# Kernel tuning notes

Measured on AMD Instinct MI355X. Metric: run time of the kernel, lower is better.

## Reference

```python
import jax, jax.numpy as jnp
import numpy as np

B, T, HID = 2, 2048, 2048
NH, DK, DV = 6, 256, 512
KEY_DIM, VAL_DIM = NH * DK, NH * DV
CONV = 4
EPS = 1e-5
SCALE = DK ** -0.5


def setup_inputs() -> dict:
    ks = jax.random.split(jax.random.key(0), 14)
    g = lambda k, shape, s=1.0: jax.random.normal(k, shape, jnp.float32) * s
    # dt_bias init as in the module: inv_dt = dt + log(-expm1(-dt))
    dt = jnp.exp(jax.random.uniform(ks[12], (NH,), jnp.float32)
                 * (np.log(0.1) - np.log(0.001)) + np.log(0.001))
    dt = jnp.clip(dt, 1e-4, None)
    inv_dt = dt + jnp.log(-jnp.expm1(-dt))
    return {
        "hidden_states": g(ks[0], (B, T, HID)),
        "w_q": g(ks[1], (HID, KEY_DIM), HID ** -0.5),
        "w_k": g(ks[2], (HID, KEY_DIM), HID ** -0.5),
        "w_v": g(ks[3], (HID, VAL_DIM), HID ** -0.5),
        "w_a": g(ks[4], (HID, NH), HID ** -0.5),
        "w_b": g(ks[5], (HID, NH), HID ** -0.5),
        "w_g": g(ks[6], (HID, VAL_DIM), HID ** -0.5),
        "w_o": g(ks[7], (VAL_DIM, HID), VAL_DIM ** -0.5),
        "conv_q": g(ks[8], (KEY_DIM, CONV), CONV ** -0.5),
        "conv_k": g(ks[9], (KEY_DIM, CONV), CONV ** -0.5),
        "conv_v": g(ks[10], (VAL_DIM, CONV), CONV ** -0.5),
        "A_log": jnp.log(jax.random.uniform(ks[11], (NH,), jnp.float32, 1e-3, 16.0)),
        "dt_bias": inv_dt,
        "norm_w": jnp.ones((DV,), jnp.float32),
    }


def short_conv(x, w):
    # depthwise causal conv1d, kernel size CONV, followed by SiLU
    K = w.shape[1]
    xp = jnp.pad(x, ((0, 0), (K - 1, 0), (0, 0)))  # left pad (causal)
    out = sum(xp[:, j:j + x.shape[1], :] * w[:, j] for j in range(K))
    return jax.nn.silu(out)


def l2norm(x):
    n = jnp.sqrt(jnp.sum(x * x, axis=-1, keepdims=True))
    return x / jnp.maximum(n, 1e-6)


def gated_delta_rule(q, k, v, glog, beta):
    # q,k: [B,T,H,DK]; v: [B,T,H,DV]; glog,beta: [B,T,H]
    # S_t = exp(g_t) (I - b_t k_t k_t^T) S_{t-1} + b_t k_t v_t^T ; o_t = scale * q_t^T S_t
    tm = lambda x: jnp.moveaxis(x, 1, 0)  # time-major

    def step(S, xs):  # S: [B,H,DK,DV]
        qt, kt, vt, gt, bt = xs
        Sd = jnp.exp(gt)[..., None, None] * S
        kS = jnp.einsum('bhk,bhkv->bhv', kt, Sd)           # k^T (a S)
        u = bt[..., None] * (vt - kS)                       # [B,H,DV]
        S_new = Sd + kt[..., None] * u[:, :, None, :]       # rank-1 update
        ot = SCALE * jnp.einsum('bhk,bhkv->bhv', qt, S_new)
        return S_new, ot

    S0 = jnp.zeros((B, NH, DK, DV), q.dtype)
    _, o = jax.lax.scan(step, S0, (tm(q), tm(k), tm(v), tm(glog), tm(beta)))
    return jnp.moveaxis(o, 0, 1)  # [B,T,H,DV]


def reference(hidden_states, w_q, w_k, w_v, w_a, w_b, w_g, w_o,
              conv_q, conv_k, conv_v, A_log, dt_bias, norm_w):
    x = hidden_states
    q = short_conv(x @ w_q, conv_q).reshape(B, T, NH, DK)
    k = short_conv(x @ w_k, conv_k).reshape(B, T, NH, DK)
    v = short_conv(x @ w_v, conv_v).reshape(B, T, NH, DV)
    beta = jax.nn.sigmoid(x @ w_b)                          # [B,T,H]
    glog = -jnp.exp(A_log) * jax.nn.softplus(x @ w_a + dt_bias)
    q = l2norm(q)
    k = l2norm(k)
    o = gated_delta_rule(q, k, v, glog, beta)               # [B,T,H,DV]
    # gated RMSNorm: rmsnorm(o) * w * silu(g_out)
    g_out = (x @ w_g).reshape(B, T, NH, DV)
    o = o * jax.lax.rsqrt(jnp.mean(o * o, axis=-1, keepdims=True) + EPS)
    o = o * norm_w * jax.nn.silu(g_out)
    return o.reshape(B, T, VAL_DIM) @ w_o
```

## Files before the change

### kernel.cpp

```cpp
#include <hip/hip_runtime.h>
#include <hip/hip_bf16.h>
#include <cstdint>

#define B_ 2
#define T_ 2048
#define HID 2048
#define NH 6
#define DK 256
#define DV 512
#define KEY_DIM (NH*DK)
#define VAL_DIM (NH*DV)
#define EPS_ 1e-5f
#define SCALE_ 0.0625f
#define MT (B_*T_)
#define CC 64
#define NC (T_/CC)

typedef __attribute__((ext_vector_type(8))) short short8;
typedef __attribute__((ext_vector_type(4))) float floatx4;
typedef __attribute__((ext_vector_type(4))) unsigned int uint4v;

union Pk8 { unsigned short us[8]; uint4v v; };

__device__ inline unsigned short f32_to_bf16(float f) {
    union { float f; unsigned int u; } v; v.f = f;
    unsigned int u = v.u;
    u += 0x7fffu + ((u >> 16) & 1u);
    return (unsigned short)(u >> 16);
}

__device__ inline float bf16_to_f32(unsigned short u) {
    union { unsigned int u; float f; } v; v.u = ((unsigned int)u) << 16;
    return v.f;
}

__device__ inline float silu_f(float x) { return x / (1.f + expf(-x)); }

__global__ __launch_bounds__(256) void cvt_bf16_kernel(const float* __restrict__ in,
                                                       unsigned short* __restrict__ out, int n) {
    int i = (blockIdx.x * 256 + threadIdx.x) * 4;
    if (i >= n) return;
    float4 v = *reinterpret_cast<const float4*>(in + i);
    ushort4 o;
    o.x = f32_to_bf16(v.x); o.y = f32_to_bf16(v.y);
    o.z = f32_to_bf16(v.z); o.w = f32_to_bf16(v.w);
    *reinterpret_cast<ushort4*>(out + i) = o;
}

__global__ __launch_bounds__(256) void transpose_cvt_kernel(const float* __restrict__ in,
                                                            unsigned short* __restrict__ out,
                                                            int K, int N) {
    __shared__ float tile[64][65];
    int k0 = blockIdx.x * 64, n0 = blockIdx.y * 64;
    int r = threadIdx.x >> 2, c0 = (threadIdx.x & 3) * 16;
    const float* src = in + (size_t)(k0 + r) * N + n0 + c0;
#pragma unroll
    for (int j = 0; j < 16; j += 4) {
        float4 v = *reinterpret_cast<const float4*>(src + j);
        tile[r][c0 + j + 0] = v.x; tile[r][c0 + j + 1] = v.y;
        tile[r][c0 + j + 2] = v.z; tile[r][c0 + j + 3] = v.w;
    }
    __syncthreads();
    int n = threadIdx.x >> 2, kc = (threadIdx.x & 3) * 16;
    unsigned short* dst = out + (size_t)(n0 + n) * K + k0 + kc;
#pragma unroll
    for (int j = 0; j < 16; j += 4) {
        ushort4 o;
        o.x = f32_to_bf16(tile[kc + j + 0][n]);
        o.y = f32_to_bf16(tile[kc + j + 1][n]);
        o.z = f32_to_bf16(tile[kc + j + 2][n]);
        o.w = f32_to_bf16(tile[kc + j + 3][n]);
        *reinterpret_cast<ushort4*>(dst + j) = o;
    }
}

#define BM 128
#define BN 128
#define BK 32
#define LDS_S 40

__global__ __launch_bounds__(256) void gemm_bf16_kernel(const unsigned short* __restrict__ A,
                                                        const unsigned short* __restrict__ BT,
                                                        float* __restrict__ C,
                                                        int M, int N, int K) {
    __shared__ __align__(16) unsigned short As[BM * LDS_S];
    __shared__ __align__(16) unsigned short Bs[BN * LDS_S];
    int tid = threadIdx.x;
    int m0 = blockIdx.y * BM, n0 = blockIdx.x * BN;
    int wave = tid >> 6, lane = tid & 63;
    int wr = (wave >> 1) * 64, wc = (wave & 1) * 64;
    int l15 = lane & 15, lh = lane >> 4;

    int srow = tid >> 1, shalf = tid & 1;
    const unsigned short* agp = A + (size_t)(m0 + srow) * K + shalf * 16;
    const unsigned short* bgp = BT + (size_t)(n0 + srow) * K + shalf * 16;
    unsigned short* asl = As + srow * LDS_S + shalf * 16;
    unsigned short* bsl = Bs + srow * LDS_S + shalf * 16;

    floatx4 acc[4][4];
#pragma unroll
    for (int m = 0; m < 4; m++)
#pragma unroll
        for (int n = 0; n < 4; n++) acc[m][n] = (floatx4){0.f, 0.f, 0.f, 0.f};

    for (int kt = 0; kt < K; kt += BK) {
        uint4v av0 = *reinterpret_cast<const uint4v*>(agp + kt);
        uint4v av1 = *reinterpret_cast<const uint4v*>(agp + kt + 8);
        uint4v bv0 = *reinterpret_cast<const uint4v*>(bgp + kt);
        uint4v bv1 = *reinterpret_cast<const uint4v*>(bgp + kt + 8);
        __syncthreads();
        *reinterpret_cast<uint4v*>(asl) = av0;
        *reinterpret_cast<uint4v*>(asl + 8) = av1;
        *reinterpret_cast<uint4v*>(bsl) = bv0;
        *reinterpret_cast<uint4v*>(bsl + 8) = bv1;
        __syncthreads();
        short8 a[4], b[4];
#pragma unroll
        for (int i = 0; i < 4; i++)
            a[i] = *reinterpret_cast<const short8*>(As + (wr + i * 16 + l15) * LDS_S + lh * 8);
#pragma unroll
        for (int i = 0; i < 4; i++)
            b[i] = *reinterpret_cast<const short8*>(Bs + (wc + i * 16 + l15) * LDS_S + lh * 8);
#pragma unroll
        for (int m = 0; m < 4; m++)
#pragma unroll
            for (int n = 0; n < 4; n++)
                acc[m][n] = __builtin_amdgcn_mfma_f32_16x16x32_bf16(a[m], b[n], acc[m][n], 0, 0, 0);
    }

#pragma unroll
    for (int m = 0; m < 4; m++)
#pragma unroll
        for (int n = 0; n < 4; n++) {
            int row = m0 + wr + m * 16 + lh * 4;
            int col = n0 + wc + n * 16 + l15;
#pragma unroll
            for (int j = 0; j < 4; j++)
                C[(size_t)(row + j) * N + col] = acc[m][n][j];
        }
}

__global__ __launch_bounds__(256) void ab_kernel(const float* __restrict__ x,
                                                 const float* __restrict__ wa,
                                                 const float* __restrict__ wb,
                                                 const float* __restrict__ A_log,
                                                 const float* __restrict__ dtb,
                                                 float* __restrict__ glog,
                                                 float* __restrict__ beta) {
    int bt = blockIdx.x, tid = threadIdx.x;
    const float* xr = x + (size_t)bt * HID;
    float pa[NH], pb[NH];
#pragma unroll
    for (int h = 0; h < NH; h++) { pa[h] = 0.f; pb[h] = 0.f; }
    for (int k = tid; k < HID; k += 256) {
        float xv = xr[k];
#pragma unroll
        for (int h = 0; h < NH; h++) {
            pa[h] = fmaf(xv, wa[k * NH + h], pa[h]);
            pb[h] = fmaf(xv, wb[k * NH + h], pb[h]);
        }
    }
    __shared__ float red[256][12];
#pragma unroll
    for (int h = 0; h < NH; h++) { red[tid][h] = pa[h]; red[tid][NH + h] = pb[h]; }
    __syncthreads();
    for (int s = 128; s > 0; s >>= 1) {
        if (tid < s)
#pragma unroll
            for (int j = 0; j < 12; j++) red[tid][j] += red[tid + s][j];
        __syncthreads();
    }
    if (tid < NH) {
        float a = red[0][tid] + dtb[tid];
        float sp = (a > 20.f) ? a : log1pf(expf(a));
        glog[(size_t)bt * NH + tid] = -expf(A_log[tid]) * sp;
        float bv = red[0][NH + tid];
        beta[(size_t)bt * NH + tid] = 1.f / (1.f + expf(-bv));
    }
}

__global__ __launch_bounds__(256) void conv_silu_l2norm_kernel(const float* __restrict__ in,
                                                               const float* __restrict__ w,
                                                               float* __restrict__ out) {
    int bt = blockIdx.x;
    int h = blockIdx.y;
    int t = bt & (T_ - 1);
    int c = h * DK + threadIdx.x;
    float4 wv = *reinterpret_cast<const float4*>(w + (size_t)c * 4);
    float acc = 0.f;
    if (t >= 3) {
        acc = in[(size_t)(bt - 3) * KEY_DIM + c] * wv.x
            + in[(size_t)(bt - 2) * KEY_DIM + c] * wv.y
            + in[(size_t)(bt - 1) * KEY_DIM + c] * wv.z
            + in[(size_t)(bt) * KEY_DIM + c] * wv.w;
    } else {
        if (t - 3 >= 0) acc = fmaf(in[(size_t)(bt - 3) * KEY_DIM + c], wv.x, acc);
        if (t - 2 >= 0) acc = fmaf(in[(size_t)(bt - 2) * KEY_DIM + c], wv.y, acc);
        if (t - 1 >= 0) acc = fmaf(in[(size_t)(bt - 1) * KEY_DIM + c], wv.z, acc);
        acc = fmaf(in[(size_t)bt * KEY_DIM + c], wv.w, acc);
    }
    float s = silu_f(acc);
    float ss = s * s;
#pragma unroll
    for (int m = 1; m < 64; m <<= 1) ss += __shfl_xor(ss, m);
    __shared__ float wsum[4];
    if ((threadIdx.x & 63) == 0) wsum[threadIdx.x >> 6] = ss;
    __syncthreads();
    float tot = wsum[0] + wsum[1] + wsum[2] + wsum[3];
    float r = 1.f / fmaxf(sqrtf(tot), 1e-6f);
    out[(size_t)bt * KEY_DIM + c] = s * r;
}

__global__ __launch_bounds__(256) void conv_silu_kernel(const float* __restrict__ in,
                                                        const float* __restrict__ w,
                                                        float* __restrict__ out) {
    int bt = blockIdx.x;
    int c = blockIdx.y * 256 + threadIdx.x;
    int t = bt & (T_ - 1);
    float4 wv = *reinterpret_cast<const float4*>(w + (size_t)c * 4);
    float acc = 0.f;
    if (t >= 3) {
        acc = in[(size_t)(bt - 3) * VAL_DIM + c] * wv.x
            + in[(size_t)(bt - 2) * VAL_DIM + c] * wv.y
            + in[(size_t)(bt - 1) * VAL_DIM + c] * wv.z
            + in[(size_t)(bt) * VAL_DIM + c] * wv.w;
    } else {
        if (t - 3 >= 0) acc = fmaf(in[(size_t)(bt - 3) * VAL_DIM + c], wv.x, acc);
        if (t - 2 >= 0) acc = fmaf(in[(size_t)(bt - 2) * VAL_DIM + c], wv.y, acc);
        if (t - 1 >= 0) acc = fmaf(in[(size_t)(bt - 1) * VAL_DIM + c], wv.z, acc);
        acc = fmaf(in[(size_t)bt * VAL_DIM + c], wv.w, acc);
    }
    out[(size_t)bt * VAL_DIM + c] = silu_f(acc);
}

__global__ __launch_bounds__(256) void chunk_prep_kernel(
    const float* __restrict__ QC, const float* __restrict__ KC, const float* __restrict__ VC,
    const float* __restrict__ GL, const float* __restrict__ BE,
    unsigned short* __restrict__ Qg, unsigned short* __restrict__ KB,
    unsigned short* __restrict__ KlT, unsigned short* __restrict__ Tm,
    unsigned short* __restrict__ Am, unsigned short* __restrict__ BVT,
    float* __restrict__ gend) {
    int c = blockIdx.x;
    int bh = blockIdx.y;
    int b = bh / NH, h = bh % NH;
    size_t idx = (size_t)bh * NC + c;
    int bt0 = b * T_ + c * CC;

    __shared__ __align__(16) char ldsbuf[64 * 264 * 2 * 2];
    unsigned short* Kb = (unsigned short*)ldsbuf;
    unsigned short* Qb = (unsigned short*)(ldsbuf + 33792);
    float* Vst = (float*)ldsbuf;
    float* Msf = (float*)(ldsbuf + 33792);
    unsigned short* Ts_lds = (unsigned short*)(ldsbuf + 50432);
    __shared__ float gc[64], es[64], bb_s[64], gtmp[64];

    int tid = threadIdx.x, wave = tid >> 6, lane = tid & 63;
    int l15 = lane & 15, lh = lane >> 4;

    if (tid < 64) {
        gtmp[tid] = GL[(size_t)(bt0 + tid) * NH + h];
        bb_s[tid] = BE[(size_t)(bt0 + tid) * NH + h];
    }

    {
        int r = tid >> 2, seg = (tid & 3) * 64;
        const float* ksrc = KC + (size_t)(bt0 + r) * KEY_DIM + h * DK + seg;
        const float* qsrc = QC + (size_t)(bt0 + r) * KEY_DIM + h * DK + seg;
#pragma unroll
        for (int jj = 0; jj < 8; jj++) {
            float4 a = *reinterpret_cast<const float4*>(ksrc + jj * 8);
            float4 a2 = *reinterpret_cast<const float4*>(ksrc + jj * 8 + 4);
            Pk8 pk;
            pk.us[0] = f32_to_bf16(a.x);  pk.us[1] = f32_to_bf16(a.y);
            pk.us[2] = f32_to_bf16(a.z);  pk.us[3] = f32_to_bf16(a.w);
            pk.us[4] = f32_to_bf16(a2.x); pk.us[5] = f32_to_bf16(a2.y);
            pk.us[6] = f32_to_bf16(a2.z); pk.us[7] = f32_to_bf16(a2.w);
            *reinterpret_cast<uint4v*>(Kb + r * 264 + seg + jj * 8) = pk.v;
            float4 qa = *reinterpret_cast<const float4*>(qsrc + jj * 8);
            float4 qa2 = *reinterpret_cast<const float4*>(qsrc + jj * 8 + 4);
            pk.us[0] = f32_to_bf16(qa.x);  pk.us[1] = f32_to_bf16(qa.y);
            pk.us[2] = f32_to_bf16(qa.z);  pk.us[3] = f32_to_bf16(qa.w);
            pk.us[4] = f32_to_bf16(qa2.x); pk.us[5] = f32_to_bf16(qa2.y);
            pk.us[6] = f32_to_bf16(qa2.z); pk.us[7] = f32_to_bf16(qa2.w);
            *reinterpret_cast<uint4v*>(Qb + r * 264 + seg + jj * 8) = pk.v;
        }
    }
    __syncthreads();

    if (wave == 0) {
        float xg = gtmp[lane];
#pragma unroll
        for (int off = 1; off < 64; off <<= 1) {
            float yg = __shfl_up(xg, off, 64);
            if (lane >= off) xg += yg;
        }
        gc[lane] = xg;
    }

    floatx4 kkf[4], qkf[4];
#pragma unroll
    for (int nt = 0; nt < 4; nt++) { kkf[nt] = (floatx4){0,0,0,0}; qkf[nt] = (floatx4){0,0,0,0}; }
#pragma unroll
    for (int kk = 0; kk < 8; kk++) {
        short8 ak = *reinterpret_cast<const short8*>(Kb + (wave * 16 + l15) * 264 + kk * 32 + lh * 8);
        short8 aq = *reinterpret_cast<const short8*>(Qb + (wave * 16 + l15) * 264 + kk * 32 + lh * 8);
#pragma unroll
        for (int nt = 0; nt < 4; nt++) {
            short8 bk = *reinterpret_cast<const short8*>(Kb + (nt * 16 + l15) * 264 + kk * 32 + lh * 8);
            kkf[nt] = __builtin_amdgcn_mfma_f32_16x16x32_bf16(ak, bk, kkf[nt], 0, 0, 0);
            qkf[nt] = __builtin_amdgcn_mfma_f32_16x16x32_bf16(aq, bk, qkf[nt], 0, 0, 0);
        }
    }
    __syncthreads();

    {
        int r = tid >> 2, seg = (tid & 3) * 64;
        float gmm = __expf(gc[r]);
        float qs = SCALE_ * gmm, ksc = bb_s[r] * gmm;
#pragma unroll
        for (int jj = 0; jj < 8; jj++) {
            Pk8 qi, ki, qo, ko;
            qi.v = *reinterpret_cast<const uint4v*>(Qb + r * 264 + seg + jj * 8);
            ki.v = *reinterpret_cast<const uint4v*>(Kb + r * 264 + seg + jj * 8);
#pragma unroll
            for (int e = 0; e < 8; e++) {
                qo.us[e] = f32_to_bf16(bf16_to_f32(qi.us[e]) * qs);
                ko.us[e] = f32_to_bf16(bf16_to_f32(ki.us[e]) * ksc);
            }
            *reinterpret_cast<uint4v*>(Qg + idx * 16384 + r * 256 + seg + jj * 8) = qo.v;
            *reinterpret_cast<uint4v*>(KB + idx * 16384 + r * 256 + seg + jj * 8) = ko.v;
        }
    }
    if (tid < 64) es[tid] = __expf(gc[63] - gc[tid]);
    __syncthreads();

#pragma unroll
    for (int nt = 0; nt < 4; nt++)
#pragma unroll
        for (int j = 0; j < 4; j++) {
            int t2 = wave * 16 + lh * 4 + j;
            int s2 = nt * 16 + l15;
            float dec = (s2 <= t2) ? __expf(gc[t2] - gc[s2]) : 0.f;
            Msf[t2 * 65 + s2] = (s2 < t2) ? bb_s[t2] * dec * kkf[nt][j] : 0.f;
            float av = (s2 <= t2) ? SCALE_ * dec * qkf[nt][j] : 0.f;
            Am[idx * 4096 + t2 * 64 + s2] = f32_to_bf16(av);
        }
    __syncthreads();

    {
        int t = lane;
        float a[16];
#pragma unroll
        for (int j2 = 0; j2 < 16; j2++) a[j2] = 0.f;
        float mcur = Msf[t * 65 + 0];
        for (int s = 0; s < 63; s++) {
            float mnext = Msf[t * 65 + s + 1];
            float m = (t > s) ? mcur : 0.f;
#pragma unroll
            for (int j2 = 0; j2 < 16; j2++) {
                int jg = 4 * j2 + wave;
                if (jg < s) {
                    float ra = __int_as_float(
                        __builtin_amdgcn_readlane(__float_as_int(a[j2]), s));
                    a[j2] = fmaf(m, -ra, a[j2]);
                } else if (jg == s) {
                    a[j2] += m;
                }
            }
            mcur = mnext;
        }
#pragma unroll
        for (int j2 = 0; j2 < 16; j2++) {
            int jg = 4 * j2 + wave;
            float v = (t == jg) ? 1.f : ((jg < t) ? -a[j2] : 0.f);
            Ts_lds[t * 72 + jg] = f32_to_bf16(v);
        }
    }
    __syncthreads();

    {
        int rr = tid >> 2, sseg = (tid & 3) * 16;
        *reinterpret_cast<uint4v*>(Tm + idx * 4096 + rr * 64 + sseg) =
            *reinterpret_cast<const uint4v*>(Ts_lds + rr * 72 + sseg);
        *reinterpret_cast<uint4v*>(Tm + idx * 4096 + rr * 64 + sseg + 8) =
            *reinterpret_cast<const uint4v*>(Ts_lds + rr * 72 + sseg + 8);
    }
    {
        int dk = tid;
#pragma unroll
        for (int sb = 0; sb < 8; sb++) {
            Pk8 pk;
#pragma unroll
            for (int e = 0; e < 8; e++) {
                int s = sb * 8 + e;
                pk.us[e] = f32_to_bf16(bf16_to_f32(Kb[s * 264 + dk]) * es[s]);
            }
            *reinterpret_cast<uint4v*>(KlT + idx * 16384 + dk * 64 + sb * 8) = pk.v;
        }
    }
    for (int hv = 0; hv < 2; hv++) {
        __syncthreads();
        int r = tid >> 2, seg = (tid & 3) * 64;
        const float* vsrc = VC + (size_t)(bt0 + r) * VAL_DIM + h * DV + hv * 256 + seg;
#pragma unroll
        for (int jj = 0; jj < 16; jj++)
            *reinterpret_cast<float4*>(Vst + r * 264 + seg + jj * 4) =
                *reinterpret_cast<const float4*>(vsrc + jj * 4);
        __syncthreads();
#pragma unroll
        for (int sb = 0; sb < 8; sb++) {
            Pk8 pk;
#pragma unroll
            for (int e = 0; e < 8; e++) {
                int s = sb * 8 + e;
                pk.us[e] = f32_to_bf16(Vst[s * 264 + tid] * bb_s[s]);
            }
            *reinterpret_cast<uint4v*>(BVT + idx * 32768 + (size_t)(hv * 256 + tid) * 64 + sb * 8) = pk.v;
        }
    }
    if (tid == 0) gend[idx] = __expf(gc[63]);
}

__global__ __launch_bounds__(256, 1) void chunk_scan_kernel(
    const unsigned short* __restrict__ Qg, const unsigned short* __restrict__ KBp,
    const unsigned short* __restrict__ KlTp, const unsigned short* __restrict__ Tmp_,
    const unsigned short* __restrict__ Amp_, const unsigned short* __restrict__ BVTp,
    const float* __restrict__ gendp, float* __restrict__ O) {
    int slice = blockIdx.x;
    int bh = blockIdx.y;
    int b = bh / NH, h = bh % NH;
    int dvbase = slice * 32;
    int tid = threadIdx.x, wave = tid >> 6, lane = tid & 63;
    int l15 = lane & 15, lh = lane >> 4;
    int ms = wave >> 1;
    int ns = wave & 1;

    __shared__ __align__(16) unsigned short QgB[64 * 264];
    __shared__ __align__(16) unsigned short KBB[64 * 264];
    __shared__ __align__(16) unsigned short KlTB[256 * 72];
    __shared__ __align__(16) unsigned short SbT[32 * 264];
    __shared__ __align__(16) unsigned short Wb[32 * 72];
    __shared__ __align__(16) unsigned short Ub[32 * 72];
    __shared__ __align__(16) float Ost[64 * 40];

    floatx4 st[8];
#pragma unroll
    for (int i = 0; i < 8; i++) st[i] = (floatx4){0.f, 0.f, 0.f, 0.f};
    for (int i = tid; i < 32 * 264; i += 256) SbT[i] = 0;

    int r = tid >> 2, seg = (tid & 3) * 64;

    for (int c = 0; c < NC; c++) {
        size_t idx = (size_t)bh * NC + c;
        const unsigned short* qg = Qg + idx * 16384;
        const unsigned short* kb = KBp + idx * 16384;
        const unsigned short* kl = KlTp + idx * 16384;
        const unsigned short* tm = Tmp_ + idx * 4096;
        const unsigned short* am = Amp_ + idx * 4096;
        const unsigned short* bvt = BVTp + idx * 32768;

        float ge = gendp[idx];
        short8 tfr[2][2], afr[2][2];
#pragma unroll
        for (int nt = 0; nt < 2; nt++)
#pragma unroll
            for (int kk = 0; kk < 2; kk++) {
                int tcol = ns * 32 + nt * 16 + l15;
                tfr[nt][kk] = *reinterpret_cast<const short8*>(tm + tcol * 64 + kk * 32 + lh * 8);
                afr[nt][kk] = *reinterpret_cast<const short8*>(am + tcol * 64 + kk * 32 + lh * 8);
            }
        float bvv[2][4];
#pragma unroll
        for (int nt = 0; nt < 2; nt++)
#pragma unroll
            for (int j = 0; j < 4; j++)
                bvv[nt][j] = bf16_to_f32(bvt[(size_t)(dvbase + ms * 16 + lh * 4 + j) * 64
                                             + ns * 32 + nt * 16 + l15]);
        uint4v qv[8], kv[8], klv[8];
#pragma unroll
        for (int j = 0; j < 8; j++) {
            qv[j] = *reinterpret_cast<const uint4v*>(qg + r * 256 + seg + j * 8);
            kv[j] = *reinterpret_cast<const uint4v*>(kb + r * 256 + seg + j * 8);
        }
#pragma unroll
        for (int j = 0; j < 8; j++)
            klv[j] = *reinterpret_cast<const uint4v*>(kl + tid * 64 + j * 8);

        __syncthreads();
#pragma unroll
        for (int j = 0; j < 8; j++) {
            *reinterpret_cast<uint4v*>(QgB + r * 264 + seg + j * 8) = qv[j];
            *reinterpret_cast<uint4v*>(KBB + r * 264 + seg + j * 8) = kv[j];
        }
#pragma unroll
        for (int j = 0; j < 8; j++)
            *reinterpret_cast<uint4v*>(KlTB + tid * 72 + j * 8) = klv[j];
        __syncthreads();

        floatx4 x2f[2], x1f[2];
#pragma unroll
        for (int nt = 0; nt < 2; nt++) { x2f[nt] = (floatx4){0,0,0,0}; x1f[nt] = (floatx4){0,0,0,0}; }
#pragma unroll
        for (int kk = 0; kk < 8; kk++) {
            short8 af = *reinterpret_cast<const short8*>(SbT + (ms * 16 + l15) * 264 + kk * 32 + lh * 8);
#pragma unroll
            for (int nt = 0; nt < 2; nt++) {
                short8 bq = *reinterpret_cast<const short8*>(QgB + (ns * 32 + nt * 16 + l15) * 264 + kk * 32 + lh * 8);
                short8 bk = *reinterpret_cast<const short8*>(KBB + (ns * 32 + nt * 16 + l15) * 264 + kk * 32 + lh * 8);
                x2f[nt] = __builtin_amdgcn_mfma_f32_16x16x32_bf16(af, bq, x2f[nt], 0, 0, 0);
                x1f[nt] = __builtin_amdgcn_mfma_f32_16x16x32_bf16(af, bk, x1f[nt], 0, 0, 0);
            }
        }
#pragma unroll
        for (int nt = 0; nt < 2; nt++)
#pragma unroll
            for (int j = 0; j < 4; j++)
                Wb[(ms * 16 + lh * 4 + j) * 72 + ns * 32 + nt * 16 + l15] =
                    f32_to_bf16(bvv[nt][j] - x1f[nt][j]);
        __syncthreads();

        floatx4 uf[2];
#pragma unroll
        for (int nt = 0; nt < 2; nt++) uf[nt] = (floatx4){0,0,0,0};
#pragma unroll
        for (int kk = 0; kk < 2; kk++) {
            short8 af = *reinterpret_cast<const short8*>(Wb + (ms * 16 + l15) * 72 + kk * 32 + lh * 8);
            uf[0] = __builtin_amdgcn_mfma_f32_16x16x32_bf16(af, tfr[0][kk], uf[0], 0, 0, 0);
            uf[1] = __builtin_amdgcn_mfma_f32_16x16x32_bf16(af, tfr[1][kk], uf[1], 0, 0, 0);
        }
#pragma unroll
        for (int nt = 0; nt < 2; nt++)
#pragma unroll
            for (int j = 0; j < 4; j++)
                Ub[(ms * 16 + lh * 4 + j) * 72 + ns * 32 + nt * 16 + l15] = f32_to_bf16(uf[nt][j]);
        __syncthreads();

#pragma unroll
        for (int i = 0; i < 8; i++) st[i] = st[i] * ge;
#pragma unroll
        for (int kk = 0; kk < 2; kk++) {
            short8 af = *reinterpret_cast<const short8*>(Ub + (ms * 16 + l15) * 72 + kk * 32 + lh * 8);
#pragma unroll
            for (int nt = 0; nt < 8; nt++) {
                short8 bf = *reinterpret_cast<const short8*>(KlTB + (ns * 128 + nt * 16 + l15) * 72 + kk * 32 + lh * 8);
                st[nt] = __builtin_amdgcn_mfma_f32_16x16x32_bf16(af, bf, st[nt], 0, 0, 0);
            }
        }
#pragma unroll
        for (int nt = 0; nt < 8; nt++)
#pragma unroll
            for (int j = 0; j < 4; j++)
                SbT[(ms * 16 + lh * 4 + j) * 264 + ns * 128 + nt * 16 + l15] = f32_to_bf16(st[nt][j]);

#pragma unroll
        for (int kk = 0; kk < 2; kk++) {
            short8 af = *reinterpret_cast<const short8*>(Ub + (ms * 16 + l15) * 72 + kk * 32 + lh * 8);
            x2f[0] = __builtin_amdgcn_mfma_f32_16x16x32_bf16(af, afr[0][kk], x2f[0], 0, 0, 0);
            x2f[1] = __builtin_amdgcn_mfma_f32_16x16x32_bf16(af, afr[1][kk], x2f[1], 0, 0, 0);
        }
#pragma unroll
        for (int nt = 0; nt < 2; nt++)
#pragma unroll
            for (int j = 0; j < 4; j++)
                Ost[(ns * 32 + nt * 16 + l15) * 40 + ms * 16 + lh * 4 + j] = x2f[nt][j];
        __syncthreads();
        int orow = tid >> 2, oseg = (tid & 3) * 8;
        float4 o0 = *reinterpret_cast<const float4*>(Ost + orow * 40 + oseg);
        float4 o1 = *reinterpret_cast<const float4*>(Ost + orow * 40 + oseg + 4);
        size_t ga = ((size_t)(b * T_ + c * CC + orow)) * VAL_DIM + h * DV + dvbase + oseg;
        *reinterpret_cast<float4*>(O + ga) = o0;
        *reinterpret_cast<float4*>(O + ga + 4) = o1;
    }
}

__global__ __launch_bounds__(256) void gated_norm_kernel(const float* __restrict__ o,
                                                         const float* __restrict__ g,
                                                         const float* __restrict__ nw,
                                                         unsigned short* __restrict__ out) {
    int bt = blockIdx.x, h = blockIdx.y, tid = threadIdx.x;
    const float* orow = o + (size_t)bt * VAL_DIM + h * DV;
    const float* grow = g + (size_t)bt * VAL_DIM + h * DV;
    float x0 = orow[tid], x1 = orow[tid + 256];
    float ss = x0 * x0 + x1 * x1;
#pragma unroll
    for (int m = 1; m < 64; m <<= 1) ss += __shfl_xor(ss, m);
    __shared__ float wsum[4];
    if ((tid & 63) == 0) wsum[tid >> 6] = ss;
    __syncthreads();
    float tot = wsum[0] + wsum[1] + wsum[2] + wsum[3];
    float r = rsqrtf(tot / (float)DV + EPS_);
    float o0 = x0 * r * nw[tid] * silu_f(grow[tid]);
    float o1 = x1 * r * nw[tid + 256] * silu_f(grow[tid + 256]);
    unsigned short* orow_o = out + (size_t)bt * VAL_DIM + h * DV;
    orow_o[tid] = f32_to_bf16(o0);
    orow_o[tid + 256] = f32_to_bf16(o1);
}

extern "C" void kernel_launch(void* const* d_in, const int* in_sizes, int n_in,
                              void* d_out, int out_size, void* d_ws, size_t ws_size,
                              hipStream_t stream) {
    const float* x     = (const float*)d_in[0];
    const float* w_q   = (const float*)d_in[1];
    const float* w_k   = (const float*)d_in[2];
    const float* w_v   = (const float*)d_in[3];
    const float* w_a   = (const float*)d_in[4];
    const float* w_b   = (const float*)d_in[5];
    const float* w_g   = (const float*)d_in[6];
    const float* w_o   = (const float*)d_in[7];
    const float* cq    = (const float*)d_in[8];
    const float* ck    = (const float*)d_in[9];
    const float* cv    = (const float*)d_in[10];
    const float* A_log = (const float*)d_in[11];
    const float* dtb   = (const float*)d_in[12];
    const float* nw    = (const float*)d_in[13];
    float* out = (float*)d_out;

    char* ws = (char*)d_ws;
    size_t off = 0;
    auto alloc = [&](size_t bytes) {
        char* p = ws + off;
        off += (bytes + 255) & ~(size_t)255;
        return p;
    };
    unsigned short* xb = (unsigned short*)alloc((size_t)MT * HID * 2);
    unsigned short* wT = (unsigned short*)alloc((size_t)VAL_DIM * HID * 2);
    float* P1 = (float*)alloc((size_t)MT * KEY_DIM * 4);
    float* QC = (float*)alloc((size_t)MT * KEY_DIM * 4);
    float* KC = (float*)alloc((size_t)MT * KEY_DIM * 4);
    float* P2 = (float*)alloc((size_t)MT * VAL_DIM * 4);
    float* VC = (float*)alloc((size_t)MT * VAL_DIM * 4);
    float* GL = (float*)alloc((size_t)MT * NH * 4);
    float* BE = (float*)alloc((size_t)MT * NH * 4);
    const int NCH = 12 * NC;
    unsigned short* KlT = (unsigned short*)alloc((size_t)NCH * 256 * 64 * 2);
    unsigned short* Tm  = (unsigned short*)alloc((size_t)NCH * 4096 * 2);
    unsigned short* Am  = (unsigned short*)alloc((size_t)NCH * 4096 * 2);
    unsigned short* BVT = (unsigned short*)alloc((size_t)NCH * 512 * 64 * 2);
    float* gend = (float*)alloc((size_t)NCH * 4);

    unsigned short* Qg = (unsigned short*)P1;
    unsigned short* KB = (unsigned short*)P1 + (size_t)NCH * 16384;
    float* OB = VC;
    unsigned short* ONB = (unsigned short*)P1;

    cvt_bf16_kernel<<<(MT * HID) / 1024, 256, 0, stream>>>(x, xb, MT * HID);

    transpose_cvt_kernel<<<dim3(HID / 64, KEY_DIM / 64), 256, 0, stream>>>(w_q, wT, HID, KEY_DIM);
    gemm_bf16_kernel<<<dim3(KEY_DIM / BN, MT / BM), 256, 0, stream>>>(xb, wT, P1, MT, KEY_DIM, HID);
    conv_silu_l2norm_kernel<<<dim3(MT, NH), 256, 0, stream>>>(P1, cq, QC);

    transpose_cvt_kernel<<<dim3(HID / 64, KEY_DIM / 64), 256, 0, stream>>>(w_k, wT, HID, KEY_DIM);
    gemm_bf16_kernel<<<dim3(KEY_DIM / BN, MT / BM), 256, 0, stream>>>(xb, wT, P1, MT, KEY_DIM, HID);
    conv_silu_l2norm_kernel<<<dim3(MT, NH), 256, 0, stream>>>(P1, ck, KC);

    transpose_cvt_kernel<<<dim3(HID / 64, VAL_DIM / 64), 256, 0, stream>>>(w_v, wT, HID, VAL_DIM);
    gemm_bf16_kernel<<<dim3(VAL_DIM / BN, MT / BM), 256, 0, stream>>>(xb, wT, P2, MT, VAL_DIM, HID);
    conv_silu_kernel<<<dim3(MT, VAL_DIM / 256), 256, 0, stream>>>(P2, cv, VC);

    transpose_cvt_kernel<<<dim3(HID / 64, VAL_DIM / 64), 256, 0, stream>>>(w_g, wT, HID, VAL_DIM);
    gemm_bf16_kernel<<<dim3(VAL_DIM / BN, MT / BM), 256, 0, stream>>>(xb, wT, P2, MT, VAL_DIM, HID);

    ab_kernel<<<MT, 256, 0, stream>>>(x, w_a, w_b, A_log, dtb, GL, BE);

    chunk_prep_kernel<<<dim3(NC, 12), 256, 0, stream>>>(QC, KC, VC, GL, BE,
                                                        Qg, KB, KlT, Tm, Am, BVT, gend);
    chunk_scan_kernel<<<dim3(16, 12), 256, 0, stream>>>(Qg, KB, KlT, Tm, Am, BVT, gend, OB);

    gated_norm_kernel<<<dim3(MT, NH), 256, 0, stream>>>(OB, P2, nw, ONB);

    transpose_cvt_kernel<<<dim3(VAL_DIM / 64, HID / 64), 256, 0, stream>>>(w_o, wT, VAL_DIM, HID);
    gemm_bf16_kernel<<<dim3(HID / BN, MT / BM), 256, 0, stream>>>(ONB, wT, out, MT, HID, VAL_DIM);
}
```

Measured before the change: 995.0 us.

## Use direct global-to-LDS loads in GEMM and restructure chunk scan per-wave

```diff
diff --git a/kernel.cpp b/kernel.cpp
--- a/kernel.cpp
+++ b/kernel.cpp
@@ -36,6 +36,12 @@
 
 __device__ inline float silu_f(float x) { return x / (1.f + expf(-x)); }
 
+__device__ inline void gl_lds16(const unsigned short* g, unsigned short* l) {
+    __builtin_amdgcn_global_load_lds(
+        (const __attribute__((address_space(1))) unsigned int*)g,
+        (__attribute__((address_space(3))) unsigned int*)l, 16, 0, 0);
+}
+
 __global__ __launch_bounds__(256) void cvt_bf16_kernel(const float* __restrict__ in,
                                                        unsigned short* __restrict__ out, int n) {
     int i = (blockIdx.x * 256 + threadIdx.x) * 4;
@@ -77,25 +83,29 @@
 #define BM 128
 #define BN 128
 #define BK 32
-#define LDS_S 40
 
 __global__ __launch_bounds__(256) void gemm_bf16_kernel(const unsigned short* __restrict__ A,
                                                         const unsigned short* __restrict__ BT,
                                                         float* __restrict__ C,
                                                         int M, int N, int K) {
-    __shared__ __align__(16) unsigned short As[BM * LDS_S];
-    __shared__ __align__(16) unsigned short Bs[BN * LDS_S];
+    __shared__ __align__(16) unsigned short As[BM * BK];
+    __shared__ __align__(16) unsigned short Bs[BN * BK];
     int tid = threadIdx.x;
     int m0 = blockIdx.y * BM, n0 = blockIdx.x * BN;
     int wave = tid >> 6, lane = tid & 63;
     int wr = (wave >> 1) * 64, wc = (wave & 1) * 64;
     int l15 = lane & 15, lh = lane >> 4;
 
-    int srow = tid >> 1, shalf = tid & 1;
-    const unsigned short* agp = A + (size_t)(m0 + srow) * K + shalf * 16;
-    const unsigned short* bgp = BT + (size_t)(n0 + srow) * K + shalf * 16;
-    unsigned short* asl = As + srow * LDS_S + shalf * 16;
-    unsigned short* bsl = Bs + srow * LDS_S + shalf * 16;
+    int srow = wave * 16 + (lane >> 2);
+    int scol = (lane & 3) * 8;
+    const unsigned short* agp0 = A + (size_t)(m0 + srow) * K + scol;
+    const unsigned short* agp1 = A + (size_t)(m0 + srow + 64) * K + scol;
+    const unsigned short* bgp0 = BT + (size_t)(n0 + srow) * K + scol;
+    const unsigned short* bgp1 = BT + (size_t)(n0 + srow + 64) * K + scol;
+    unsigned short* asl0 = As + wave * 512;
+    unsigned short* asl1 = As + 2048 + wave * 512;
+    unsigned short* bsl0 = Bs + wave * 512;
+    unsigned short* bsl1 = Bs + 2048 + wave * 512;
 
     floatx4 acc[4][4];
 #pragma unroll
@@ -104,23 +114,19 @@
         for (int n = 0; n < 4; n++) acc[m][n] = (floatx4){0.f, 0.f, 0.f, 0.f};
 
     for (int kt = 0; kt < K; kt += BK) {
-        uint4v av0 = *reinterpret_cast<const uint4v*>(agp + kt);
-        uint4v av1 = *reinterpret_cast<const uint4v*>(agp + kt + 8);
-        uint4v bv0 = *reinterpret_cast<const uint4v*>(bgp + kt);
-        uint4v bv1 = *reinterpret_cast<const uint4v*>(bgp + kt + 8);
         __syncthreads();
-        *reinterpret_cast<uint4v*>(asl) = av0;
-        *reinterpret_cast<uint4v*>(asl + 8) = av1;
-        *reinterpret_cast<uint4v*>(bsl) = bv0;
-        *reinterpret_cast<uint4v*>(bsl + 8) = bv1;
+        gl_lds16(agp0 + kt, asl0);
+        gl_lds16(agp1 + kt, asl1);
+        gl_lds16(bgp0 + kt, bsl0);
+        gl_lds16(bgp1 + kt, bsl1);
         __syncthreads();
         short8 a[4], b[4];
 #pragma unroll
         for (int i = 0; i < 4; i++)
-            a[i] = *reinterpret_cast<const short8*>(As + (wr + i * 16 + l15) * LDS_S + lh * 8);
+            a[i] = *reinterpret_cast<const short8*>(As + (wr + i * 16 + l15) * BK + lh * 8);
 #pragma unroll
         for (int i = 0; i < 4; i++)
-            b[i] = *reinterpret_cast<const short8*>(Bs + (wc + i * 16 + l15) * LDS_S + lh * 8);
+            b[i] = *reinterpret_cast<const short8*>(Bs + (wc + i * 16 + l15) * BK + lh * 8);
 #pragma unroll
         for (int m = 0; m < 4; m++)
 #pragma unroll
@@ -421,7 +427,7 @@
     if (tid == 0) gend[idx] = __expf(gc[63]);
 }
 
-__global__ __launch_bounds__(256, 1) void chunk_scan_kernel(
+__global__ __launch_bounds__(128, 1) void chunk_scan_kernel(
     const unsigned short* __restrict__ Qg, const unsigned short* __restrict__ KBp,
     const unsigned short* __restrict__ KlTp, const unsigned short* __restrict__ Tmp_,
     const unsigned short* __restrict__ Amp_, const unsigned short* __restrict__ BVTp,
@@ -429,147 +435,176 @@
     int slice = blockIdx.x;
     int bh = blockIdx.y;
     int b = bh / NH, h = bh % NH;
-    int dvbase = slice * 32;
     int tid = threadIdx.x, wave = tid >> 6, lane = tid & 63;
     int l15 = lane & 15, lh = lane >> 4;
-    int ms = wave >> 1;
-    int ns = wave & 1;
+    int dvbase = slice * 32 + wave * 16;
 
     __shared__ __align__(16) unsigned short QgB[64 * 264];
     __shared__ __align__(16) unsigned short KBB[64 * 264];
     __shared__ __align__(16) unsigned short KlTB[256 * 72];
-    __shared__ __align__(16) unsigned short SbT[32 * 264];
-    __shared__ __align__(16) unsigned short Wb[32 * 72];
-    __shared__ __align__(16) unsigned short Ub[32 * 72];
-    __shared__ __align__(16) float Ost[64 * 40];
-
-    floatx4 st[8];
-#pragma unroll
-    for (int i = 0; i < 8; i++) st[i] = (floatx4){0.f, 0.f, 0.f, 0.f};
-    for (int i = tid; i < 32 * 264; i += 256) SbT[i] = 0;
-
-    int r = tid >> 2, seg = (tid & 3) * 64;
+    __shared__ __align__(16) unsigned short SbT[2][16 * 264];
+    __shared__ __align__(16) unsigned short Wb[2][16 * 72];
+    __shared__ __align__(16) unsigned short Ub[2][16 * 72];
+    __shared__ __align__(16) float Ost[2][64 * 20];
+
+    unsigned short* sbt = SbT[wave];
+    unsigned short* wb  = Wb[wave];
+    unsigned short* ub  = Ub[wave];
+    float* ost = Ost[wave];
+
+    floatx4 st[16];
+#pragma unroll
+    for (int i = 0; i < 16; i++) st[i] = (floatx4){0.f, 0.f, 0.f, 0.f};
+    for (int i = lane; i < 16 * 264; i += 64) sbt[i] = 0;
+
+    int r = tid >> 1, seg = (tid & 1) * 128;
+    size_t idx0 = (size_t)bh * NC;
+
+    uint4v qv[16], kv[16], klv[16];
+    {
+        const unsigned short* qg = Qg + idx0 * 16384;
+        const unsigned short* kb = KBp + idx0 * 16384;
+        const unsigned short* kl = KlTp + idx0 * 16384;
+#pragma unroll
+        for (int j = 0; j < 16; j++) {
+            qv[j] = *reinterpret_cast<const uint4v*>(qg + r * 256 + seg + j * 8);
+            kv[j] = *reinterpret_cast<const uint4v*>(kb + r * 256 + seg + j * 8);
+        }
+#pragma unroll
+        for (int j = 0; j < 8; j++) {
+            klv[j]     = *reinterpret_cast<const uint4v*>(kl + tid * 64 + j * 8);
+            klv[j + 8] = *reinterpret_cast<const uint4v*>(kl + (tid + 128) * 64 + j * 8);
+        }
+    }
 
     for (int c = 0; c < NC; c++) {
-        size_t idx = (size_t)bh * NC + c;
-        const unsigned short* qg = Qg + idx * 16384;
-        const unsigned short* kb = KBp + idx * 16384;
-        const unsigned short* kl = KlTp + idx * 16384;
+        size_t idx = idx0 + c;
         const unsigned short* tm = Tmp_ + idx * 4096;
         const unsigned short* am = Amp_ + idx * 4096;
         const unsigned short* bvt = BVTp + idx * 32768;
-
         float ge = gendp[idx];
-        short8 tfr[2][2], afr[2][2];
-#pragma unroll
-        for (int nt = 0; nt < 2; nt++)
-#pragma unroll
-            for (int kk = 0; kk < 2; kk++) {
-                int tcol = ns * 32 + nt * 16 + l15;
-                tfr[nt][kk] = *reinterpret_cast<const short8*>(tm + tcol * 64 + kk * 32 + lh * 8);
-                afr[nt][kk] = *reinterpret_cast<const short8*>(am + tcol * 64 + kk * 32 + lh * 8);
-            }
-        float bvv[2][4];
-#pragma unroll
-        for (int nt = 0; nt < 2; nt++)
-#pragma unroll
-            for (int j = 0; j < 4; j++)
-                bvv[nt][j] = bf16_to_f32(bvt[(size_t)(dvbase + ms * 16 + lh * 4 + j) * 64
-                                             + ns * 32 + nt * 16 + l15]);
-        uint4v qv[8], kv[8], klv[8];
-#pragma unroll
-        for (int j = 0; j < 8; j++) {
-            qv[j] = *reinterpret_cast<const uint4v*>(qg + r * 256 + seg + j * 8);
-            kv[j] = *reinterpret_cast<const uint4v*>(kb + r * 256 + seg + j * 8);
-        }
-#pragma unroll
-        for (int j = 0; j < 8; j++)
-            klv[j] = *reinterpret_cast<const uint4v*>(kl + tid * 64 + j * 8);
 
         __syncthreads();
 #pragma unroll
-        for (int j = 0; j < 8; j++) {
+        for (int j = 0; j < 16; j++) {
             *reinterpret_cast<uint4v*>(QgB + r * 264 + seg + j * 8) = qv[j];
             *reinterpret_cast<uint4v*>(KBB + r * 264 + seg + j * 8) = kv[j];
         }
 #pragma unroll
-        for (int j = 0; j < 8; j++)
+        for (int j = 0; j < 8; j++) {
             *reinterpret_cast<uint4v*>(KlTB + tid * 72 + j * 8) = klv[j];
+            *reinterpret_cast<uint4v*>(KlTB + (tid + 128) * 72 + j * 8) = klv[j + 8];
+        }
         __syncthreads();
 
-        floatx4 x2f[2], x1f[2];
-#pragma unroll
-        for (int nt = 0; nt < 2; nt++) { x2f[nt] = (floatx4){0,0,0,0}; x1f[nt] = (floatx4){0,0,0,0}; }
+        if (c + 1 < NC) {
+            const unsigned short* qg2 = Qg + (idx + 1) * 16384;
+            const unsigned short* kb2 = KBp + (idx + 1) * 16384;
+            const unsigned short* kl2 = KlTp + (idx + 1) * 16384;
+#pragma unroll
+            for (int j = 0; j < 16; j++) {
+                qv[j] = *reinterpret_cast<const uint4v*>(qg2 + r * 256 + seg + j * 8);
+                kv[j] = *reinterpret_cast<const uint4v*>(kb2 + r * 256 + seg + j * 8);
+            }
+#pragma unroll
+            for (int j = 0; j < 8; j++) {
+                klv[j]     = *reinterpret_cast<const uint4v*>(kl2 + tid * 64 + j * 8);
+                klv[j + 8] = *reinterpret_cast<const uint4v*>(kl2 + (tid + 128) * 64 + j * 8);
+            }
+        }
+
+        short8 tfr[4][2], afr[4][2];
+#pragma unroll
+        for (int nt = 0; nt < 4; nt++)
+#pragma unroll
+            for (int kk = 0; kk < 2; kk++) {
+                tfr[nt][kk] = *reinterpret_cast<const short8*>(tm + (nt * 16 + l15) * 64 + kk * 32 + lh * 8);
+                afr[nt][kk] = *reinterpret_cast<const short8*>(am + (nt * 16 + l15) * 64 + kk * 32 + lh * 8);
+            }
+        float bvv[4][4];
+#pragma unroll
+        for (int nt = 0; nt < 4; nt++)
+#pragma unroll
+            for (int j = 0; j < 4; j++)
+                bvv[nt][j] = bf16_to_f32(bvt[(size_t)(dvbase + lh * 4 + j) * 64 + nt * 16 + l15]);
+
+        floatx4 x2f[4], x1f[4];
+#pragma unroll
+        for (int nt = 0; nt < 4; nt++) { x2f[nt] = (floatx4){0,0,0,0}; x1f[nt] = (floatx4){0,0,0,0}; }
 #pragma unroll
         for (int kk = 0; kk < 8; kk++) {
-            short8 af = *reinterpret_cast<const short8*>(SbT + (ms * 16 + l15) * 264 + kk * 32 + lh * 8);
-#pragma unroll
-            for (int nt = 0; nt < 2; nt++) {
-                short8 bq = *reinterpret_cast<const short8*>(QgB + (ns * 32 + nt * 16 + l15) * 264 + kk * 32 + lh * 8);
-                short8 bk = *reinterpret_cast<const short8*>(KBB + (ns * 32 + nt * 16 + l15) * 264 + kk * 32 + lh * 8);
+            short8 af = *reinterpret_cast<const short8*>(sbt + l15 * 264 + kk * 32 + lh * 8);
+#pragma unroll
+            for (int nt = 0; nt < 4; nt++) {
+                short8 bq = *reinterpret_cast<const short8*>(QgB + (nt * 16 + l15) * 264 + kk * 32 + lh * 8);
+                short8 bk = *reinterpret_cast<const short8*>(KBB + (nt * 16 + l15) * 264 + kk * 32 + lh * 8);
                 x2f[nt] = __builtin_amdgcn_mfma_f32_16x16x32_bf16(af, bq, x2f[nt], 0, 0, 0);
                 x1f[nt] = __builtin_amdgcn_mfma_f32_16x16x32_bf16(af, bk, x1f[nt], 0, 0, 0);
             }
         }
-#pragma unroll
-        for (int nt = 0; nt < 2; nt++)
+
+#pragma unroll
+        for (int nt = 0; nt < 4; nt++)
 #pragma unroll
             for (int j = 0; j < 4; j++)
-                Wb[(ms * 16 + lh * 4 + j) * 72 + ns * 32 + nt * 16 + l15] =
-                    f32_to_bf16(bvv[nt][j] - x1f[nt][j]);
-        __syncthreads();
-
-        floatx4 uf[2];
-#pragma unroll
-        for (int nt = 0; nt < 2; nt++) uf[nt] = (floatx4){0,0,0,0};
+                wb[(lh * 4 + j) * 72 + nt * 16 + l15] = f32_to_bf16(bvv[nt][j] - x1f[nt][j]);
+
+        floatx4 uf[4];
+#pragma unroll
+        for (int nt = 0; nt < 4; nt++) uf[nt] = (floatx4){0,0,0,0};
 #pragma unroll
         for (int kk = 0; kk < 2; kk++) {
-            short8 af = *reinterpret_cast<const short8*>(Wb + (ms * 16 + l15) * 72 + kk * 32 + lh * 8);
-            uf[0] = __builtin_amdgcn_mfma_f32_16x16x32_bf16(af, tfr[0][kk], uf[0], 0, 0, 0);
-            uf[1] = __builtin_amdgcn_mfma_f32_16x16x32_bf16(af, tfr[1][kk], uf[1], 0, 0, 0);
-        }
-#pragma unroll
-        for (int nt = 0; nt < 2; nt++)
+            short8 af = *reinterpret_cast<const short8*>(wb + l15 * 72 + kk * 32 + lh * 8);
+#pragma unroll
+            for (int nt = 0; nt < 4; nt++)
+                uf[nt] = __builtin_amdgcn_mfma_f32_16x16x32_bf16(af, tfr[nt][kk], uf[nt], 0, 0, 0);
+        }
+#pragma unroll
+        for (int nt = 0; nt < 4; nt++)
 #pragma unroll
             for (int j = 0; j < 4; j++)
-                Ub[(ms * 16 + lh * 4 + j) * 72 + ns * 32 + nt * 16 + l15] = f32_to_bf16(uf[nt][j]);
-        __syncthreads();
-
-#pragma unroll
-        for (int i = 0; i < 8; i++) st[i] = st[i] * ge;
+                ub[(lh * 4 + j) * 72 + nt * 16 + l15] = f32_to_bf16(uf[nt][j]);
+
+#pragma unroll
+        for (int i = 0; i < 16; i++) st[i] = st[i] * ge;
 #pragma unroll
         for (int kk = 0; kk < 2; kk++) {
-            short8 af = *reinterpret_cast<const short8*>(Ub + (ms * 16 + l15) * 72 + kk * 32 + lh * 8);
-#pragma unroll
-            for (int nt = 0; nt < 8; nt++) {
-                short8 bf = *reinterpret_cast<const short8*>(KlTB + (ns * 128 + nt * 16 + l15) * 72 + kk * 32 + lh * 8);
-                st[nt] = __builtin_amdgcn_mfma_f32_16x16x32_bf16(af, bf, st[nt], 0, 0, 0);
-            }
-        }
-#pragma unroll
-        for (int nt = 0; nt < 8; nt++)
+            short8 af = *reinterpret_cast<const short8*>(ub + l15 * 72 + kk * 32 + lh * 8);
+#pragma unroll
+            for (int dkt = 0; dkt < 16; dkt++) {
+                short8 bf = *reinterpret_cast<const short8*>(KlTB + (dkt * 16 + l15) * 72 + kk * 32 + lh * 8);
+                st[dkt] = __builtin_amdgcn_mfma_f32_16x16x32_bf16(af, bf, st[dkt], 0, 0, 0);
+            }
+        }
+#pragma unroll
+        for (int dkt = 0; dkt < 16; dkt++)
 #pragma unroll
             for (int j = 0; j < 4; j++)
-                SbT[(ms * 16 + lh * 4 + j) * 264 + ns * 128 + nt * 16 + l15] = f32_to_bf16(st[nt][j]);
+                sbt[(lh * 4 + j) * 264 + dkt * 16 + l15] = f32_to_bf16(st[dkt][j]);
 
 #pragma unroll
         for (int kk = 0; kk < 2; kk++) {
-            short8 af = *reinterpret_cast<const short8*>(Ub + (ms * 16 + l15) * 72 + kk * 32 + lh * 8);
-            x2f[0] = __builtin_amdgcn_mfma_f32_16x16x32_bf16(af, afr[0][kk], x2f[0], 0, 0, 0);
-            x2f[1] = __builtin_amdgcn_mfma_f32_16x16x32_bf16(af, afr[1][kk], x2f[1], 0, 0, 0);
-        }
-#pragma unroll
-        for (int nt = 0; nt < 2; nt++)
+            short8 af = *reinterpret_cast<const short8*>(ub + l15 * 72 + kk * 32 + lh * 8);
+#pragma unroll
+            for (int nt = 0; nt < 4; nt++)
+                x2f[nt] = __builtin_amdgcn_mfma_f32_16x16x32_bf16(af, afr[nt][kk], x2f[nt], 0, 0, 0);
+        }
+#pragma unroll
+        for (int nt = 0; nt < 4; nt++)
 #pragma unroll
             for (int j = 0; j < 4; j++)
-                Ost[(ns * 32 + nt * 16 + l15) * 40 + ms * 16 + lh * 4 + j] = x2f[nt][j];
-        __syncthreads();
-        int orow = tid >> 2, oseg = (tid & 3) * 8;
-        float4 o0 = *reinterpret_cast<const float4*>(Ost + orow * 40 + oseg);
-        float4 o1 = *reinterpret_cast<const float4*>(Ost + orow * 40 + oseg + 4);
-        size_t ga = ((size_t)(b * T_ + c * CC + orow)) * VAL_DIM + h * DV + dvbase + oseg;
-        *reinterpret_cast<float4*>(O + ga) = o0;
-        *reinterpret_cast<float4*>(O + ga + 4) = o1;
+                ost[(nt * 16 + l15) * 20 + lh * 4 + j] = x2f[nt][j];
+        {
+            float4 o0 = *reinterpret_cast<const float4*>(ost + lane * 20);
+            float4 o1 = *reinterpret_cast<const float4*>(ost + lane * 20 + 4);
+            float4 o2 = *reinterpret_cast<const float4*>(ost + lane * 20 + 8);
+            float4 o3 = *reinterpret_cast<const float4*>(ost + lane * 20 + 12);
+            size_t ga = ((size_t)(b * T_ + c * CC + lane)) * VAL_DIM + h * DV + dvbase;
+            *reinterpret_cast<float4*>(O + ga)      = o0;
+            *reinterpret_cast<float4*>(O + ga + 4)  = o1;
+            *reinterpret_cast<float4*>(O + ga + 8)  = o2;
+            *reinterpret_cast<float4*>(O + ga + 12) = o3;
+        }
     }
 }
 
@@ -664,7 +699,7 @@
 
     chunk_prep_kernel<<<dim3(NC, 12), 256, 0, stream>>>(QC, KC, VC, GL, BE,
                                                         Qg, KB, KlT, Tm, Am, BVT, gend);
-    chunk_scan_kernel<<<dim3(16, 12), 256, 0, stream>>>(Qg, KB, KlT, Tm, Am, BVT, gend, OB);
+    chunk_scan_kernel<<<dim3(16, 12), 128, 0, stream>>>(Qg, KB, KlT, Tm, Am, BVT, gend, OB);
 
     gated_norm_kernel<<<dim3(MT, NH), 256, 0, stream>>>(OB, P2, nw, ONB);
 
```

Measured after the change: 1.056 ms. +6.1%, slower.
